# Kernel tuning notes

Measured on AMD Instinct MI355X. Metric: run time of the kernel, lower is better.

The kernel has to match this reference:

```python
import jax, jax.numpy as jnp
import numpy as np

B, N = 8, 8192
S_ATTN, S_NONE = 128, 384          # npoint = (npoint_all=512, npoint_none_attn=384) -> npoint_attn=128
S = S_ATTN + S_NONE
NSAMPLE = 64
RADIUS = 0.4
D_FEAT = 64
MLP = [64, 64, 128]
IN_CH = 3 + D_FEAT


def fps(pts, K):
    # pytorch3d.sample_farthest_points, start index 0, full lengths. pts: [B,N,3]
    B_, N_, _ = pts.shape
    def body(carry, _):
        min_d2, last = carry
        lp = jnp.take_along_axis(pts, last[:, None, None], axis=1)      # [B,1,3]
        d2 = jnp.sum((pts - lp) ** 2, -1)                               # [B,N]
        min_d2 = jnp.minimum(min_d2, d2)
        nxt = jnp.argmax(min_d2, -1).astype(jnp.int32)
        return (min_d2, nxt), last
    init = (jnp.full((B_, N_), jnp.float32(1e10)), jnp.zeros((B_,), jnp.int32))
    _, idxs = jax.lax.scan(body, init, None, length=K)
    idxs = idxs.T                                                       # [B,K]
    sampled = jnp.take_along_axis(pts, idxs[..., None], axis=1)         # [B,K,3]
    return sampled, idxs


def ball_query(query, pts, K, radius):
    # pytorch3d.ball_query: first K points with d2 < r^2 in index order; idx pad=-1, nn pad=0.
    d2 = jnp.sum((query[:, :, None, :] - pts[:, None, :, :]) ** 2, -1)  # [B,S,N]
    mask = d2 < radius * radius
    order = jnp.cumsum(mask.astype(jnp.int32), -1) - 1
    slot = jnp.where(mask & (order < K), order, K)                      # overflow -> dump slot K
    n_ids = jnp.broadcast_to(jnp.arange(pts.shape[1], dtype=jnp.int32), slot.shape)
    def scatter_row(slot_row, ids_row):
        return jnp.full((K + 1,), -1, jnp.int32).at[slot_row].set(ids_row)[:K]
    idx = jax.vmap(jax.vmap(scatter_row))(slot, n_ids)                  # [B,S,K]
    valid = idx >= 0
    gathered = jax.vmap(lambda p, i: p[i])(pts, jnp.where(valid, idx, 0))  # [B,S,K,3]
    nn = jnp.where(valid[..., None], gathered, 0.0)
    return idx, nn


def _forward(xyz, points, attention, ws, bs):
    xyz_t = xyz.transpose(0, 2, 1)            # [B,N,3]
    pts_t = points.transpose(0, 2, 1)         # [B,N,D]
    attn_t = attention.transpose(0, 2, 1)     # [B,N,1]

    attn_xyz = attn_t * xyz_t
    none_xyz = (1.0 - attn_t) * xyz_t
    new_attn_xyz, idx_a = fps(attn_xyz, S_ATTN)
    new_none_xyz, idx_n = fps(none_xyz, S_NONE)
    new_xyz = jnp.concatenate([new_attn_xyz, new_none_xyz], axis=1)     # [B,S,3]
    fps_idx = jnp.concatenate([idx_a, idx_n], axis=1)                   # [B,S]
    new_attention = jnp.take_along_axis(attn_t, fps_idx[..., None], axis=1)  # [B,S,1]

    idx, grouped_xyz = ball_query(new_xyz, xyz_t, NSAMPLE, RADIUS)
    grouped_norm = grouped_xyz - new_xyz[:, :, None, :]                 # [B,S,K,3]
    gather_idx = jnp.where(idx < 0, N - 1, idx)   # torch index -1 wraps to last point
    grouped_pts = jax.vmap(lambda p, i: p[i])(pts_t, gather_idx)        # [B,S,K,D]
    feat = jnp.concatenate([grouped_norm, grouped_pts], -1)             # [B,S,K,3+D]

    x = feat.transpose(0, 3, 2, 1)                                      # [B,C,K,S]
    for w, b in zip(ws, bs):                                            # 1x1 Conv2d + ReLU
        x = jax.nn.relu(jnp.einsum('oc,bcks->boks', w, x) + b[None, :, None, None])
    new_points = jnp.max(x, axis=2)                                     # MaxPool over nsample -> [B,C',S]
    return new_xyz.transpose(0, 2, 1), new_points, new_attention.transpose(0, 2, 1)


def setup_inputs() -> dict:
    key = jax.random.key(0)
    ks = jax.random.split(key, 8)
    xyz = jax.random.normal(ks[0], (B, 3, N), jnp.float32)
    points = jax.random.normal(ks[1], (B, D_FEAT, N), jnp.float32)
    attention = jnp.round(jax.random.uniform(ks[2], (B, 1, N), jnp.float32))  # 0/1 mask
    inp = {'xyz': xyz, 'points': points, 'attention': attention}
    last = IN_CH
    for i, oc in enumerate(MLP):
        inp[f'w{i}'] = jax.random.normal(ks[3 + i], (oc, last), jnp.float32) / np.float32(np.sqrt(last))
        inp[f'b{i}'] = jnp.zeros((oc,), jnp.float32)
        last = oc
    return inp


def reference(xyz, points, attention, w0, b0, w1, b1, w2, b2):
    return _forward(xyz, points, attention, (w0, w1, w2), (b0, b1, b2))
```

## Files before the change

### kernel.cpp

```cpp
#include <hip/hip_runtime.h>
#include <cstdint>
#include <cstddef>

#define NB 8
#define NPTS 8192
#define S_TOT 512
#define NSAMP 64
#define DFEAT 64
#define INCH 67
#define SLOTS 17
#define CCAP (SLOTS * 256)

typedef __attribute__((ext_vector_type(8))) short v8s;
typedef __attribute__((ext_vector_type(4))) short v4s;
typedef __attribute__((ext_vector_type(4))) float v4f;

__device__ __forceinline__ float d2_exact(float ax, float ay, float az,
                                          float bx, float by, float bz) {
    float dx = __fsub_rn(ax, bx);
    float dy = __fsub_rn(ay, by);
    float dz = __fsub_rn(az, bz);
    return __fadd_rn(__fadd_rn(__fmul_rn(dx, dx), __fmul_rn(dy, dy)), __fmul_rn(dz, dz));
}

__device__ __forceinline__ unsigned short f2b(float f) {
    unsigned u = __float_as_uint(f);
    return (unsigned short)((u + 0x7fffu + ((u >> 16) & 1u)) >> 16);
}

template <int CTRL>
__device__ __forceinline__ unsigned long long dpp_max_u64(unsigned long long k) {
    int lo = (int)(unsigned)(k & 0xffffffffull);
    int hi = (int)(unsigned)(k >> 32);
    int slo = __builtin_amdgcn_update_dpp(lo, lo, CTRL, 0xf, 0xf, false);
    int shi = __builtin_amdgcn_update_dpp(hi, hi, CTRL, 0xf, 0xf, false);
    unsigned long long o = ((unsigned long long)(unsigned)shi << 32) | (unsigned)slo;
    return (o > k) ? o : k;
}

__global__ __launch_bounds__(1024) void fps_compact(
    const float* __restrict__ xyz, const float* __restrict__ attn,
    float4* __restrict__ cxyz, int* __restrict__ hdr)
{
    int blk = blockIdx.x;
    int b = blk >> 1, grp = blk & 1;
    const float* xb = xyz + (size_t)b * 3 * NPTS;
    const float* ab = attn + (size_t)b * NPTS;
    float4* c4 = cxyz + (size_t)blk * CCAP;

    int tid = threadIdx.x, lane = tid & 63, wid = tid >> 6;
    int n0 = tid * 8;

    __shared__ int s_repmin;
    __shared__ int s_ws[16];
    if (tid == 0) s_repmin = NPTS;
    __syncthreads();

    float av[8];
    *(float4*)&av[0] = *(const float4*)(ab + n0);
    *(float4*)&av[4] = *(const float4*)(ab + n0 + 4);
    int cnt = 0, mymin = NPTS;
    bool keep[8];
#pragma unroll
    for (int j = 0; j < 8; j++) {
        keep[j] = grp ? (av[j] == 0.0f) : (av[j] != 0.0f);
        cnt += keep[j] ? 1 : 0;
        if (!keep[j] && n0 + j < mymin) mymin = n0 + j;
    }
    if (mymin < NPTS) atomicMin(&s_repmin, mymin);

    int incl = cnt;
#pragma unroll
    for (int off = 1; off <= 32; off <<= 1) {
        int t = __shfl_up(incl, off);
        if (lane >= off) incl += t;
    }
    if (lane == 63) s_ws[wid] = incl;
    __syncthreads();
    int woff = 0, tot = 0;
#pragma unroll
    for (int w = 0; w < 16; w++) { if (w < wid) woff += s_ws[w]; tot += s_ws[w]; }
    int pos = woff + incl - cnt;
    int rm = s_repmin;
    int rm_eff = (rm < NPTS) ? rm : 0x7fffffff;

    float xv[8], yv[8], zv[8];
    *(float4*)&xv[0] = *(const float4*)(xb + n0);
    *(float4*)&xv[4] = *(const float4*)(xb + n0 + 4);
    *(float4*)&yv[0] = *(const float4*)(xb + NPTS + n0);
    *(float4*)&yv[4] = *(const float4*)(xb + NPTS + n0 + 4);
    *(float4*)&zv[0] = *(const float4*)(xb + 2 * NPTS + n0);
    *(float4*)&zv[4] = *(const float4*)(xb + 2 * NPTS + n0 + 4);
#pragma unroll
    for (int j = 0; j < 8; j++) {
        if (keep[j]) {
            int fin = pos + ((n0 + j > rm_eff) ? 1 : 0);
            if (fin < CCAP)
                c4[fin] = make_float4(xv[j], yv[j], zv[j], 0.0f);
            pos++;
        }
    }
    if (tid == 0) {
        int M = tot;
        if (rm < NPTS) {
            if (rm < CCAP)
                c4[rm] = make_float4(__fmul_rn(0.0f, xb[rm]),
                                     __fmul_rn(0.0f, xb[NPTS + rm]),
                                     __fmul_rn(0.0f, xb[2 * NPTS + rm]), 0.0f);
            M++;
        }
        hdr[blk * 2] = M;
        hdr[blk * 2 + 1] = (rm < NPTS) ? rm : -1;
    }
}

__global__ __launch_bounds__(256, 1) void fps_fused(
    const float* __restrict__ attn,
    const float4* __restrict__ cxyz,
    const int* __restrict__ hdr,
    float* __restrict__ out0, float* __restrict__ out2,
    const float* __restrict__ pts, unsigned short* __restrict__ ptsTh,
    const float* __restrict__ w0, const float* __restrict__ w1,
    const float* __restrict__ w2, unsigned short* __restrict__ wp)
{
    __shared__ __align__(16) char smem[69632 + 6144 + 64];
    int blk = blockIdx.x;
    int tid = threadIdx.x;

    if (blk < 16) {
        int b = blk >> 1, grp = blk & 1;
        int K = grp ? 384 : 128;
        int soff = grp ? 128 : 0;
        int M = hdr[blk * 2];
        int repslot = hdr[blk * 2 + 1];
        if (M > CCAP) return;
        int lane = tid & 63, wid = tid >> 6;

        const float4* cb = cxyz + (size_t)blk * CCAP;
        float4* sc = (float4*)smem;
        float4* s_obuf = (float4*)(smem + 69632);
        unsigned long long* s_red = (unsigned long long*)(smem + 69632 + 6144);

        float px[SLOTS], py[SLOTS], pz[SLOTS], md[SLOTS];
#pragma unroll
        for (int i = 0; i < SLOTS; i++) {
            int sl = i * 256 + tid;
            bool v = sl < M;
            float4 c = v ? cb[sl] : make_float4(0.f, 0.f, 0.f, 0.f);
            px[i] = c.x; py[i] = c.y; pz[i] = c.z;
            sc[sl] = c;
            md[i] = v ? 1e10f : -1.0f;
        }
        float4 c0 = cb[0];
        float lx = c0.x, ly = c0.y, lz = c0.z;
        float a_last = attn[(size_t)b * NPTS];
        float kept_a = grp ? 0.0f : 1.0f;
        float rep_a  = grp ? 1.0f : 0.0f;

        for (int k = 0; k < K; k++) {
            if (tid == 0) s_obuf[k] = make_float4(lx, ly, lz, a_last);
            if (k == K - 1) break;

            float bv = -1.0f; int bslot = 0x7fffffff;
#pragma unroll
            for (int i = 0; i < SLOTS; i++) {
                float d2 = d2_exact(px[i], py[i], pz[i], lx, ly, lz);
                md[i] = fminf(md[i], d2);
                int sl = i * 256 + tid;
                bool w = (md[i] > bv) || ((md[i] == bv) && (sl < bslot));
                bv = w ? md[i] : bv;
                bslot = w ? sl : bslot;
            }
            unsigned long long key = (bv >= 0.0f)
                ? (((unsigned long long)__float_as_uint(bv) << 32) | (unsigned)(~bslot))
                : 0ull;
            key = dpp_max_u64<0x111>(key);
            key = dpp_max_u64<0x112>(key);
            key = dpp_max_u64<0x114>(key);
            key = dpp_max_u64<0x118>(key);
            key = dpp_max_u64<0x142>(key);
            key = dpp_max_u64<0x143>(key);
            int buf = k & 1;
            if (lane == 63) s_red[buf * 4 + wid] = key;
            __syncthreads();

            const unsigned long long* rp = &s_red[buf * 4];
            unsigned long long k0 = rp[0], k1 = rp[1], k2 = rp[2], k3 = rp[3];
            unsigned long long m01 = (k0 > k1) ? k0 : k1;
            unsigned long long m23 = (k2 > k3) ? k2 : k3;
            unsigned long long g = (m01 > m23) ? m01 : m23;
            int wslot = (int)(~(unsigned)g);
            float4 wc = sc[wslot];
            lx = wc.x; ly = wc.y; lz = wc.z;
            a_last = (wslot == repslot) ? rep_a : kept_a;
        }
        __syncthreads();
        for (int k2i = tid; k2i < K; k2i += 256) {
            float4 o = s_obuf[k2i];
            int sg = soff + k2i;
            out0[(size_t)b * 3 * S_TOT + sg] = o.x;
            out0[(size_t)b * 3 * S_TOT + S_TOT + sg] = o.y;
            out0[(size_t)b * 3 * S_TOT + 2 * S_TOT + sg] = o.z;
            out2[(size_t)b * S_TOT + sg] = o.w;
        }
    } else if (blk < 16 + 1024) {
        float (*t)[65] = (float(*)[65])smem;
        int blk2 = blk - 16;
        int b = blk2 >> 7;
        int n0 = (blk2 & 127) * 64;
        int tx = tid & 63, ty = tid >> 6;
        for (int c = ty; c < 64; c += 4)
            t[c][tx] = pts[((size_t)b * DFEAT + c) * NPTS + n0 + tx];
        __syncthreads();
        for (int r = ty; r < 64; r += 4)
            ptsTh[((size_t)b * NPTS + n0 + r) * DFEAT + tx] = f2b(t[tx][r]);
    } else if (tid < 64) {
        int t = blk - (16 + 1024), l = tid;
        int kq = (l >> 4) * 8, n16 = l & 15;
        unsigned short o[8];
#pragma unroll
        for (int j = 0; j < 8; j++) {
            float v;
            if (t < 12) {
                int kt = t >> 2, nt = t & 3;
                int k = kt * 32 + kq + j, n = nt * 16 + n16;
                v = (k < 64) ? w0[n * INCH + 3 + k] : (k < 67 ? w0[n * INCH + (k - 64)] : 0.0f);
            } else if (t < 20) {
                int tt = t - 12, kt = tt >> 2, nt = tt & 3;
                v = w1[(nt * 16 + n16) * 64 + kt * 32 + kq + j];
            } else {
                int tt = t - 20, kt = tt >> 3, nt = tt & 7;
                v = w2[(nt * 16 + n16) * 64 + kt * 32 + kq + j];
            }
            o[j] = f2b(v);
        }
        *(v8s*)&wp[(size_t)t * 512 + l * 8] = *(v8s*)o;
    }
}

__global__ __launch_bounds__(1024, 1) void fps_kernel(
    const float* __restrict__ xyz, const float* __restrict__ attn,
    const int* __restrict__ hdr,
    float* __restrict__ out0, float* __restrict__ out2)
{
    int blk = blockIdx.x;
    if (hdr != nullptr && hdr[blk * 2] <= CCAP) return;
    int b = blk >> 1, grp = blk & 1;
    int K = grp ? 384 : 128;
    int soff = grp ? 128 : 0;
    int tid = threadIdx.x, lane = tid & 63, wid = tid >> 6;
    const float* xb = xyz + (size_t)b * 3 * NPTS;
    const float* ab = attn + (size_t)b * NPTS;

    float px[8], py[8], pz[8], md[8];
#pragma unroll
    for (int i = 0; i < 8; i++) {
        int n = tid + i * 1024;
        float a = ab[n];
        float f = grp ? __fsub_rn(1.0f, a) : a;
        px[i] = __fmul_rn(f, xb[n]);
        py[i] = __fmul_rn(f, xb[NPTS + n]);
        pz[i] = __fmul_rn(f, xb[2 * NPTS + n]);
        md[i] = 1e10f;
    }
    __shared__ unsigned long long s_red[2][16];
    float a_last = ab[0];
    float f0 = grp ? __fsub_rn(1.0f, a_last) : a_last;
    float lx = __fmul_rn(f0, xb[0]);
    float ly = __fmul_rn(f0, xb[NPTS]);
    float lz = __fmul_rn(f0, xb[2 * NPTS]);

    for (int k = 0; k < K; k++) {
        if (tid == 0) {
            int sg = soff + k;
            out0[(size_t)b * 3 * S_TOT + sg] = lx;
            out0[(size_t)b * 3 * S_TOT + S_TOT + sg] = ly;
            out0[(size_t)b * 3 * S_TOT + 2 * S_TOT + sg] = lz;
            out2[(size_t)b * S_TOT + sg] = a_last;
        }
        if (k == K - 1) break;
        float bv = -1.0f; int bi = 0;
#pragma unroll
        for (int i = 0; i < 8; i++) {
            float d2 = d2_exact(px[i], py[i], pz[i], lx, ly, lz);
            md[i] = fminf(md[i], d2);
            if (md[i] > bv) { bv = md[i]; bi = tid + i * 1024; }
        }
        unsigned long long best =
            ((unsigned long long)__float_as_uint(bv) << 32) | (unsigned)(~bi);
#pragma unroll
        for (int off = 32; off >= 1; off >>= 1) {
            unsigned long long o = __shfl_down(best, off);
            best = (o > best) ? o : best;
        }
        if (lane == 0) s_red[k & 1][wid] = best;
        __syncthreads();
        unsigned long long r = (lane < 16) ? s_red[k & 1][lane] : 0ull;
#pragma unroll
        for (int off = 8; off >= 1; off >>= 1) {
            unsigned long long o = __shfl_down(r, off);
            r = (o > r) ? o : r;
        }
        r = __shfl(r, 0);
        int n = (int)(~(unsigned)r);
        a_last = ab[n];
        float fl = grp ? __fsub_rn(1.0f, a_last) : a_last;
        lx = __fmul_rn(fl, xb[n]);
        ly = __fmul_rn(fl, xb[NPTS + n]);
        lz = __fmul_rn(fl, xb[2 * NPTS + n]);
    }
}

__global__ __launch_bounds__(64, 2) void ball_mlp_mfma(
    const float* __restrict__ xyz,
    const unsigned short* __restrict__ ptsTh,
    const unsigned short* __restrict__ wp,
    const float* __restrict__ b0, const float* __restrict__ b1,
    const float* __restrict__ b2,
    const float* __restrict__ out0,
    float* __restrict__ out1)
{
    const float R2 = (float)(0.4 * 0.4);
    int q = blockIdx.x;
    int b = q >> 9;
    int sg = q & 511;
    int lane = threadIdx.x;
    int col = lane & 15, quad = lane >> 4, kq = quad * 8;

    const float* xb = xyz + (size_t)b * 3 * NPTS;
    float qx = out0[(size_t)b * 3 * S_TOT + sg];
    float qy = out0[(size_t)b * 3 * S_TOT + S_TOT + sg];
    float qz = out0[(size_t)b * 3 * S_TOT + 2 * S_TOT + sg];

    __shared__ int s_idx[NSAMP];
    __shared__ __align__(16) short sBuf[64 * 104];
    unsigned long long* s_mask = (unsigned long long*)sBuf;

#pragma unroll 8
    for (int j = 0; j < 128; j++) {
        int n = j * 64 + lane;
        float d2 = d2_exact(qx, qy, qz, xb[n], xb[NPTS + n], xb[2 * NPTS + n]);
        unsigned long long m = __ballot(d2 < R2);
        if (lane == 0) s_mask[j] = m;
    }

    unsigned long long m0 = s_mask[lane];
    unsigned long long m1 = s_mask[64 + lane];
    int c0 = (int)__popcll(m0), c1 = (int)__popcll(m1);
    int i0 = c0;
#pragma unroll
    for (int off = 1; off <= 32; off <<= 1) {
        int t = __shfl_up(i0, off);
        if (lane >= off) i0 += t;
    }
    int T0 = __shfl(i0, 63);
    int i1 = c1;
#pragma unroll
    for (int off = 1; off <= 32; off <<= 1) {
        int t = __shfl_up(i1, off);
        if (lane >= off) i1 += t;
    }
    int total = T0 + __shfl(i1, 63);
    int p0 = i0 - c0;
    int p1 = T0 + i1 - c1;

    {
        int base = p0, org = lane * 64;
        while (m0 && base < NSAMP) {
            int bp = __ffsll((long long)m0) - 1;
            s_idx[base++] = org + bp;
            m0 &= m0 - 1;
        }
        base = p1; org = (64 + lane) * 64;
        while (m1 && base < NSAMP) {
            int bp = __ffsll((long long)m1) - 1;
            s_idx[base++] = org + bp;
            m1 &= m1 - 1;
        }
    }
    int cnt = (total > NSAMP) ? NSAMP : total;

    int nb = (lane < cnt) ? s_idx[lane] : -1;
    float nx_ = 0.f, ny_ = 0.f, nz_ = 0.f;
    if (nb >= 0) { nx_ = xb[nb]; ny_ = xb[NPTS + nb]; nz_ = xb[2 * NPTS + nb]; }
    float fx = nx_ - qx, fy = ny_ - qy, fz = nz_ - qz;
    int row = (nb < 0) ? (NPTS - 1) : nb;

    {
        const unsigned short* ph = ptsTh + ((size_t)b * NPTS + row) * DFEAT;
        short* xr = &sBuf[lane * 104];
#pragma unroll
        for (int i = 0; i < 8; i++)
            *(v8s*)(xr + i * 8) = *(const v8s*)(ph + i * 8);
#pragma unroll
        for (int i = 0; i < 5; i++)
            *(v8s*)(xr + 64 + i * 8) = (v8s)0;
        v4s xyzp;
        xyzp[0] = (short)f2b(fx); xyzp[1] = (short)f2b(fy);
        xyzp[2] = (short)f2b(fz); xyzp[3] = 0;
        *(v4s*)(xr + 64) = xyzp;
    }

    const v8s* wpv = (const v8s*)wp;

    v4f acc[4][4];
#pragma unroll
    for (int nt = 0; nt < 4; nt++) {
        float bb = b0[nt * 16 + col];
#pragma unroll
        for (int mt = 0; mt < 4; mt++) acc[mt][nt] = (v4f){bb, bb, bb, bb};
    }
#pragma unroll
    for (int kt = 0; kt < 3; kt++) {
        v8s bf[4];
#pragma unroll
        for (int nt = 0; nt < 4; nt++) bf[nt] = wpv[(kt * 4 + nt) * 64 + lane];
#pragma unroll
        for (int mt = 0; mt < 4; mt++) {
            v8s a = *(const v8s*)&sBuf[(mt * 16 + col) * 104 + kt * 32 + kq];
#pragma unroll
            for (int nt = 0; nt < 4; nt++)
                acc[mt][nt] = __builtin_amdgcn_mfma_f32_16x16x32_bf16(a, bf[nt], acc[mt][nt], 0, 0, 0);
        }
    }
#pragma unroll
    for (int mt = 0; mt < 4; mt++)
#pragma unroll
        for (int nt = 0; nt < 4; nt++)
#pragma unroll
            for (int r = 0; r < 4; r++)
                sBuf[(mt * 16 + quad * 4 + r) * 72 + nt * 16 + col] =
                    (short)f2b(fmaxf(acc[mt][nt][r], 0.0f));

#pragma unroll
    for (int nt = 0; nt < 4; nt++) {
        float bb = b1[nt * 16 + col];
#pragma unroll
        for (int mt = 0; mt < 4; mt++) acc[mt][nt] = (v4f){bb, bb, bb, bb};
    }
#pragma unroll
    for (int kt = 0; kt < 2; kt++) {
        v8s bf[4];
#pragma unroll
        for (int nt = 0; nt < 4; nt++) bf[nt] = wpv[(12 + kt * 4 + nt) * 64 + lane];
#pragma unroll
        for (int mt = 0; mt < 4; mt++) {
            v8s a = *(const v8s*)&sBuf[(mt * 16 + col) * 72 + kt * 32 + kq];
#pragma unroll
            for (int nt = 0; nt < 4; nt++)
                acc[mt][nt] = __builtin_amdgcn_mfma_f32_16x16x32_bf16(a, bf[nt], acc[mt][nt], 0, 0, 0);
        }
    }
#pragma unroll
    for (int mt = 0; mt < 4; mt++)
#pragma unroll
        for (int nt = 0; nt < 4; nt++)
#pragma unroll
            for (int r = 0; r < 4; r++)
                sBuf[(mt * 16 + quad * 4 + r) * 72 + nt * 16 + col] =
                    (short)f2b(fmaxf(acc[mt][nt][r], 0.0f));

#pragma unroll
    for (int p = 0; p < 2; p++) {
#pragma unroll
        for (int nt = 0; nt < 4; nt++) {
            float bb = b2[(p * 4 + nt) * 16 + col];
#pragma unroll
            for (int mt = 0; mt < 4; mt++) acc[mt][nt] = (v4f){bb, bb, bb, bb};
        }
#pragma unroll
        for (int kt = 0; kt < 2; kt++) {
            v8s bf[4];
#pragma unroll
            for (int nt = 0; nt < 4; nt++)
                bf[nt] = wpv[(20 + kt * 8 + p * 4 + nt) * 64 + lane];
#pragma unroll
            for (int mt = 0; mt < 4; mt++) {
                v8s a = *(const v8s*)&sBuf[(mt * 16 + col) * 72 + kt * 32 + kq];
#pragma unroll
                for (int nt = 0; nt < 4; nt++)
                    acc[mt][nt] = __builtin_amdgcn_mfma_f32_16x16x32_bf16(a, bf[nt], acc[mt][nt], 0, 0, 0);
            }
        }
#pragma unroll
        for (int nt = 0; nt < 4; nt++) {
            float v = 0.0f;
#pragma unroll
            for (int mt = 0; mt < 4; mt++)
#pragma unroll
                for (int r = 0; r < 4; r++)
                    v = fmaxf(v, acc[mt][nt][r]);
            v = fmaxf(v, __shfl_xor(v, 16));
            v = fmaxf(v, __shfl_xor(v, 32));
            if (lane < 16)
                out1[((size_t)(b * 128 + (p * 4 + nt) * 16 + lane)) * S_TOT + sg] = v;
        }
    }
}

__global__ __launch_bounds__(64, 1) void ball_mlp_fb(
    const float* __restrict__ xyz, const float* __restrict__ pts,
    const float* __restrict__ w0, const float* __restrict__ b0,
    const float* __restrict__ w1, const float* __restrict__ b1,
    const float* __restrict__ w2, const float* __restrict__ b2,
    const float* __restrict__ out0, float* __restrict__ out1)
{
    const float R2 = (float)(0.4 * 0.4);
    int q = blockIdx.x;
    int b = q >> 9, sg = q & 511, lane = threadIdx.x;
    const float* xb = xyz + (size_t)b * 3 * NPTS;
    float qx = out0[(size_t)b * 3 * S_TOT + sg];
    float qy = out0[(size_t)b * 3 * S_TOT + S_TOT + sg];
    float qz = out0[(size_t)b * 3 * S_TOT + 2 * S_TOT + sg];

    __shared__ int s_idx[NSAMP];
    __shared__ float s_h[32 * 64];
    int cnt = 0;
    for (int base = 0; base < NPTS; base += 64) {
        int n = base + lane;
        float d2 = d2_exact(qx, qy, qz, xb[n], xb[NPTS + n], xb[2 * NPTS + n]);
        bool flag = d2 < R2;
        unsigned long long m = __ballot(flag);
        int pos = cnt + (int)__popcll(m & ((1ull << lane) - 1ull));
        if (flag && pos < NSAMP) s_idx[pos] = n;
        cnt += (int)__popcll(m);
    }
    if (cnt > NSAMP) cnt = NSAMP;
    int nb = (lane < cnt) ? s_idx[lane] : -1;
    float nx_ = 0.f, ny_ = 0.f, nz_ = 0.f;
    if (nb >= 0) { nx_ = xb[nb]; ny_ = xb[NPTS + nb]; nz_ = xb[2 * NPTS + nb]; }
    float fx = nx_ - qx, fy = ny_ - qy, fz = nz_ - qz;
    int row = (nb < 0) ? (NPTS - 1) : nb;

    float h1[64];
#pragma unroll
    for (int o = 0; o < 64; o++) {
        float a = __builtin_fmaf(w0[o * INCH + 0], fx, b0[o]);
        a = __builtin_fmaf(w0[o * INCH + 1], fy, a);
        h1[o] = __builtin_fmaf(w0[o * INCH + 2], fz, a);
    }
    const float* pb = pts + (size_t)b * DFEAT * NPTS + row;
#pragma unroll 1
    for (int c = 0; c < 64; c++) {
        float f = pb[(size_t)c * NPTS];
#pragma unroll
        for (int o = 0; o < 64; o++)
            h1[o] = __builtin_fmaf(w0[o * INCH + 3 + c], f, h1[o]);
    }
#pragma unroll
    for (int c = 0; c < 32; c++) s_h[c * 64 + lane] = fmaxf(h1[c], 0.0f);
    float h1h[32];
#pragma unroll
    for (int c = 0; c < 32; c++) h1h[c] = fmaxf(h1[32 + c], 0.0f);

    float h2[64];
#pragma unroll
    for (int o = 0; o < 64; o++) h2[o] = b1[o];
#pragma unroll 1
    for (int c = 0; c < 32; c++) {
        float hc = s_h[c * 64 + lane];
#pragma unroll
        for (int o = 0; o < 64; o++)
            h2[o] = __builtin_fmaf(w1[o * 64 + c], hc, h2[o]);
    }
#pragma unroll
    for (int c = 0; c < 32; c++) s_h[c * 64 + lane] = h1h[c];
#pragma unroll 1
    for (int c = 0; c < 32; c++) {
        float hc = s_h[c * 64 + lane];
#pragma unroll
        for (int o = 0; o < 64; o++)
            h2[o] = __builtin_fmaf(w1[o * 64 + (32 + c)], hc, h2[o]);
    }
#pragma unroll
    for (int o = 0; o < 64; o++) h2[o] = fmaxf(h2[o], 0.0f);

#pragma unroll 2
    for (int o = 0; o < 128; o++) {
        const float* wr = w2 + o * 64;
        float acc = b2[o];
#pragma unroll
        for (int c = 0; c < 64; c++) acc = __builtin_fmaf(wr[c], h2[c], acc);
        acc = fmaxf(acc, 0.0f);
#pragma unroll
        for (int off = 32; off >= 1; off >>= 1)
            acc = fmaxf(acc, __shfl_down(acc, off));
        if (lane == 0) out1[((size_t)(b * 128 + o)) * S_TOT + sg] = acc;
    }
}

extern "C" void kernel_launch(void* const* d_in, const int* in_sizes, int n_in,
                              void* d_out, int out_size, void* d_ws, size_t ws_size,
                              hipStream_t stream) {
    const float* xyz  = (const float*)d_in[0];
    const float* pts  = (const float*)d_in[1];
    const float* attn = (const float*)d_in[2];
    const float* w0 = (const float*)d_in[3];
    const float* b0 = (const float*)d_in[4];
    const float* w1 = (const float*)d_in[5];
    const float* b1 = (const float*)d_in[6];
    const float* w2 = (const float*)d_in[7];
    const float* b2 = (const float*)d_in[8];

    float* out0 = (float*)d_out;
    float* out1 = out0 + (size_t)NB * 3 * S_TOT;
    float* out2 = out1 + (size_t)NB * 128 * S_TOT;

    unsigned short* wp    = (unsigned short*)d_ws;
    unsigned short* ptsTh = (unsigned short*)((char*)d_ws + 36864);
    float4*         cxyz  = (float4*)((char*)d_ws + 36864 + 8388608);
    int*            hdr   = (int*)((char*)cxyz + (size_t)16 * CCAP * 16);
    const size_t need = 36864 + 8388608 + (size_t)16 * CCAP * 16 + 128;

    if (ws_size >= need) {
        fps_compact<<<16, 1024, 0, stream>>>(xyz, attn, cxyz, hdr);
        fps_fused<<<16 + 1024 + 36, 256, 0, stream>>>(
            attn, cxyz, hdr, out0, out2, pts, ptsTh, w0, w1, w2, wp);
        fps_kernel<<<16, 1024, 0, stream>>>(xyz, attn, hdr, out0, out2);
        ball_mlp_mfma<<<NB * S_TOT, 64, 0, stream>>>(xyz, ptsTh, wp, b0, b1, b2,
                                                     out0, out1);
    } else {
        fps_kernel<<<16, 1024, 0, stream>>>(xyz, attn, nullptr, out0, out2);
        ball_mlp_fb<<<NB * S_TOT, 64, 0, stream>>>(xyz, pts, w0, b0, w1, b1,
                                                   w2, b2, out0, out1);
    }
}
```

Baseline: 630.7 us.

## Overlap ball-query MLP with FPS via progress flags in fused kernel

Appends 1024 consumer blocks to the fused FPS kernel. FPS blocks publish sampled centroids every 16 iterations through release fences and per-block progress counters. Consumer warps spin on those counters and on a transpose/weight-pack completion count, then run ball query plus the MFMA MLP for their centroid while FPS continues. A timeout marks queries as skipped so a tail kernel recomputes them, which guards against deadlock when consumers cannot be co-resident with producers, at the cost of spin-wait overhead and raised FPS wave priority.

```diff
diff --git a/kernel.cpp b/kernel.cpp
--- a/kernel.cpp
+++ b/kernel.cpp
@@ -10,6 +10,8 @@
 #define INCH 67
 #define SLOTS 17
 #define CCAP (SLOTS * 256)
+#define TDONE 1060
+#define BALLW 13568
 
 typedef __attribute__((ext_vector_type(8))) short v8s;
 typedef __attribute__((ext_vector_type(4))) short v4s;
@@ -38,17 +40,205 @@
     return (o > k) ? o : k;
 }
 
+__device__ __forceinline__ void ball_one(
+    const float* __restrict__ xyz,
+    const unsigned short* __restrict__ ptsTh,
+    const unsigned short* __restrict__ wp,
+    const float* __restrict__ b0, const float* __restrict__ b1,
+    const float* __restrict__ b2,
+    const float* __restrict__ out0, float* __restrict__ out1,
+    int b, int sg, int lane, short* sBuf, int* s_idx)
+{
+    const float R2 = (float)(0.4 * 0.4);
+    int col = lane & 15, quad = lane >> 4, kq = quad * 8;
+
+    const float* xb = xyz + (size_t)b * 3 * NPTS;
+    float qx = out0[(size_t)b * 3 * S_TOT + sg];
+    float qy = out0[(size_t)b * 3 * S_TOT + S_TOT + sg];
+    float qz = out0[(size_t)b * 3 * S_TOT + 2 * S_TOT + sg];
+
+    unsigned long long* s_mask = (unsigned long long*)sBuf;
+
+#pragma unroll 8
+    for (int j = 0; j < 128; j++) {
+        int n = j * 64 + lane;
+        float d2 = d2_exact(qx, qy, qz, xb[n], xb[NPTS + n], xb[2 * NPTS + n]);
+        unsigned long long m = __ballot(d2 < R2);
+        if (lane == 0) s_mask[j] = m;
+    }
+
+    unsigned long long m0 = s_mask[lane];
+    unsigned long long m1 = s_mask[64 + lane];
+    int c0 = (int)__popcll(m0), c1 = (int)__popcll(m1);
+    int i0 = c0;
+#pragma unroll
+    for (int off = 1; off <= 32; off <<= 1) {
+        int t = __shfl_up(i0, off);
+        if (lane >= off) i0 += t;
+    }
+    int T0 = __shfl(i0, 63);
+    int i1 = c1;
+#pragma unroll
+    for (int off = 1; off <= 32; off <<= 1) {
+        int t = __shfl_up(i1, off);
+        if (lane >= off) i1 += t;
+    }
+    int total = T0 + __shfl(i1, 63);
+    int p0 = i0 - c0;
+    int p1 = T0 + i1 - c1;
+
+    {
+        int base = p0, org = lane * 64;
+        while (m0 && base < NSAMP) {
+            int bp = __ffsll((long long)m0) - 1;
+            s_idx[base++] = org + bp;
+            m0 &= m0 - 1;
+        }
+        base = p1; org = (64 + lane) * 64;
+        while (m1 && base < NSAMP) {
+            int bp = __ffsll((long long)m1) - 1;
+            s_idx[base++] = org + bp;
+            m1 &= m1 - 1;
+        }
+    }
+    int cnt = (total > NSAMP) ? NSAMP : total;
+
+    int nb = (lane < cnt) ? s_idx[lane] : -1;
+    float nx_ = 0.f, ny_ = 0.f, nz_ = 0.f;
+    if (nb >= 0) { nx_ = xb[nb]; ny_ = xb[NPTS + nb]; nz_ = xb[2 * NPTS + nb]; }
+    float fx = nx_ - qx, fy = ny_ - qy, fz = nz_ - qz;
+    int row = (nb < 0) ? (NPTS - 1) : nb;
+
+    {
+        const unsigned short* ph = ptsTh + ((size_t)b * NPTS + row) * DFEAT;
+        short* xr = &sBuf[lane * 104];
+#pragma unroll
+        for (int i = 0; i < 8; i++)
+            *(v8s*)(xr + i * 8) = *(const v8s*)(ph + i * 8);
+#pragma unroll
+        for (int i = 0; i < 5; i++)
+            *(v8s*)(xr + 64 + i * 8) = (v8s)0;
+        v4s xyzp;
+        xyzp[0] = (short)f2b(fx); xyzp[1] = (short)f2b(fy);
+        xyzp[2] = (short)f2b(fz); xyzp[3] = 0;
+        *(v4s*)(xr + 64) = xyzp;
+    }
+
+    const v8s* wpv = (const v8s*)wp;
+
+    v4f acc[4][4];
+#pragma unroll
+    for (int nt = 0; nt < 4; nt++) {
+        float bb = b0[nt * 16 + col];
+#pragma unroll
+        for (int mt = 0; mt < 4; mt++) acc[mt][nt] = (v4f){bb, bb, bb, bb};
+    }
+#pragma unroll
+    for (int kt = 0; kt < 3; kt++) {
+        v8s bf[4];
+#pragma unroll
+        for (int nt = 0; nt < 4; nt++) bf[nt] = wpv[(kt * 4 + nt) * 64 + lane];
+#pragma unroll
+        for (int mt = 0; mt < 4; mt++) {
+            v8s a = *(const v8s*)&sBuf[(mt * 16 + col) * 104 + kt * 32 + kq];
+#pragma unroll
+            for (int nt = 0; nt < 4; nt++)
+                acc[mt][nt] = __builtin_amdgcn_mfma_f32_16x16x32_bf16(a, bf[nt], acc[mt][nt], 0, 0, 0);
+        }
+    }
+#pragma unroll
+    for (int mt = 0; mt < 4; mt++)
+#pragma unroll
+        for (int nt = 0; nt < 4; nt++)
+#pragma unroll
+            for (int r = 0; r < 4; r++)
+                sBuf[(mt * 16 + quad * 4 + r) * 72 + nt * 16 + col] =
+                    (short)f2b(fmaxf(acc[mt][nt][r], 0.0f));
+
+#pragma unroll
+    for (int nt = 0; nt < 4; nt++) {
+        float bb = b1[nt * 16 + col];
+#pragma unroll
+        for (int mt = 0; mt < 4; mt++) acc[mt][nt] = (v4f){bb, bb, bb, bb};
+    }
+#pragma unroll
+    for (int kt = 0; kt < 2; kt++) {
+        v8s bf[4];
+#pragma unroll
+        for (int nt = 0; nt < 4; nt++) bf[nt] = wpv[(12 + kt * 4 + nt) * 64 + lane];
+#pragma unroll
+        for (int mt = 0; mt < 4; mt++) {
+            v8s a = *(const v8s*)&sBuf[(mt * 16 + col) * 72 + kt * 32 + kq];
+#pragma unroll
+            for (int nt = 0; nt < 4; nt++)
+                acc[mt][nt] = __builtin_amdgcn_mfma_f32_16x16x32_bf16(a, bf[nt], acc[mt][nt], 0, 0, 0);
+        }
+    }
+#pragma unroll
+    for (int mt = 0; mt < 4; mt++)
+#pragma unroll
+        for (int nt = 0; nt < 4; nt++)
+#pragma unroll
+            for (int r = 0; r < 4; r++)
+                sBuf[(mt * 16 + quad * 4 + r) * 72 + nt * 16 + col] =
+                    (short)f2b(fmaxf(acc[mt][nt][r], 0.0f));
+
+#pragma unroll
+    for (int p = 0; p < 2; p++) {
+#pragma unroll
+        for (int nt = 0; nt < 4; nt++) {
+            float bb = b2[(p * 4 + nt) * 16 + col];
+#pragma unroll
+            for (int mt = 0; mt < 4; mt++) acc[mt][nt] = (v4f){bb, bb, bb, bb};
+        }
+#pragma unroll
+        for (int kt = 0; kt < 2; kt++) {
+            v8s bf[4];
+#pragma unroll
+            for (int nt = 0; nt < 4; nt++)
+                bf[nt] = wpv[(20 + kt * 8 + p * 4 + nt) * 64 + lane];
+#pragma unroll
+            for (int mt = 0; mt < 4; mt++) {
+                v8s a = *(const v8s*)&sBuf[(mt * 16 + col) * 72 + kt * 32 + kq];
+#pragma unroll
+                for (int nt = 0; nt < 4; nt++)
+                    acc[mt][nt] = __builtin_amdgcn_mfma_f32_16x16x32_bf16(a, bf[nt], acc[mt][nt], 0, 0, 0);
+            }
+        }
+#pragma unroll
+        for (int nt = 0; nt < 4; nt++) {
+            float v = 0.0f;
+#pragma unroll
+            for (int mt = 0; mt < 4; mt++)
+#pragma unroll
+                for (int r = 0; r < 4; r++)
+                    v = fmaxf(v, acc[mt][nt][r]);
+            v = fmaxf(v, __shfl_xor(v, 16));
+            v = fmaxf(v, __shfl_xor(v, 32));
+            if (lane < 16)
+                out1[((size_t)(b * 128 + (p * 4 + nt) * 16 + lane)) * S_TOT + sg] = v;
+        }
+    }
+}
+
 __global__ __launch_bounds__(1024) void fps_compact(
     const float* __restrict__ xyz, const float* __restrict__ attn,
-    float4* __restrict__ cxyz, int* __restrict__ hdr)
+    float4* __restrict__ cxyz, int* __restrict__ hdr,
+    int* __restrict__ prog, int* __restrict__ tcount, int* __restrict__ skip)
 {
     int blk = blockIdx.x;
+    int tid = threadIdx.x;
+    if (blk == 0) {
+        if (tid < 16) prog[tid] = 0;
+        if (tid == 16) tcount[0] = 0;
+        ((int4*)skip)[tid] = make_int4(0, 0, 0, 0);
+    }
     int b = blk >> 1, grp = blk & 1;
     const float* xb = xyz + (size_t)b * 3 * NPTS;
     const float* ab = attn + (size_t)b * NPTS;
     float4* c4 = cxyz + (size_t)blk * CCAP;
 
-    int tid = threadIdx.x, lane = tid & 63, wid = tid >> 6;
+    int lane = tid & 63, wid = tid >> 6;
     int n0 = tid * 8;
 
     __shared__ int s_repmin;
@@ -121,7 +311,12 @@
     float* __restrict__ out0, float* __restrict__ out2,
     const float* __restrict__ pts, unsigned short* __restrict__ ptsTh,
     const float* __restrict__ w0, const float* __restrict__ w1,
-    const float* __restrict__ w2, unsigned short* __restrict__ wp)
+    const float* __restrict__ w2, unsigned short* __restrict__ wp,
+    const float* __restrict__ xyz,
+    const float* __restrict__ b0v, const float* __restrict__ b1v,
+    const float* __restrict__ b2v,
+    float* __restrict__ out1,
+    int* __restrict__ prog, int* __restrict__ tcount, int* __restrict__ skip)
 {
     __shared__ __align__(16) char smem[69632 + 6144 + 64];
     int blk = blockIdx.x;
@@ -133,8 +328,13 @@
         int soff = grp ? 128 : 0;
         int M = hdr[blk * 2];
         int repslot = hdr[blk * 2 + 1];
-        if (M > CCAP) return;
+        if (M > CCAP) {
+            if (tid == 0)
+                __hip_atomic_store(&prog[blk], -1, __ATOMIC_RELAXED, __HIP_MEMORY_SCOPE_AGENT);
+            return;
+        }
         int lane = tid & 63, wid = tid >> 6;
+        __builtin_amdgcn_s_setprio(1);
 
         const float4* cb = cxyz + (size_t)blk * CCAP;
         float4* sc = (float4*)smem;
@@ -193,15 +393,38 @@
             float4 wc = sc[wslot];
             lx = wc.x; ly = wc.y; lz = wc.z;
             a_last = (wslot == repslot) ? rep_a : kept_a;
+
+            if (((k & 15) == 15) && wid == 3) {
+                if (lane < 16) {
+                    int kk = k - 15 + lane;
+                    float4 o = s_obuf[kk];
+                    int sgO = soff + kk;
+                    size_t base = (size_t)b * 3 * S_TOT;
+                    out0[base + sgO] = o.x;
+                    out0[base + S_TOT + sgO] = o.y;
+                    out0[base + 2 * S_TOT + sgO] = o.z;
+                    out2[(size_t)b * S_TOT + sgO] = o.w;
+                }
+                __builtin_amdgcn_fence(__ATOMIC_RELEASE, "agent");
+                if (lane == 0)
+                    __hip_atomic_store(&prog[blk], k + 1, __ATOMIC_RELAXED, __HIP_MEMORY_SCOPE_AGENT);
+            }
         }
         __syncthreads();
-        for (int k2i = tid; k2i < K; k2i += 256) {
-            float4 o = s_obuf[k2i];
-            int sg = soff + k2i;
-            out0[(size_t)b * 3 * S_TOT + sg] = o.x;
-            out0[(size_t)b * 3 * S_TOT + S_TOT + sg] = o.y;
-            out0[(size_t)b * 3 * S_TOT + 2 * S_TOT + sg] = o.z;
-            out2[(size_t)b * S_TOT + sg] = o.w;
+        if (wid == 3) {
+            if (lane < 16) {
+                int kk = K - 16 + lane;
+                float4 o = s_obuf[kk];
+                int sgO = soff + kk;
+                size_t base = (size_t)b * 3 * S_TOT;
+                out0[base + sgO] = o.x;
+                out0[base + S_TOT + sgO] = o.y;
+                out0[base + 2 * S_TOT + sgO] = o.z;
+                out2[(size_t)b * S_TOT + sgO] = o.w;
+            }
+            __builtin_amdgcn_fence(__ATOMIC_RELEASE, "agent");
+            if (lane == 0)
+                __hip_atomic_store(&prog[blk], K, __ATOMIC_RELAXED, __HIP_MEMORY_SCOPE_AGENT);
         }
     } else if (blk < 16 + 1024) {
         float (*t)[65] = (float(*)[65])smem;
@@ -214,27 +437,68 @@
         __syncthreads();
         for (int r = ty; r < 64; r += 4)
             ptsTh[((size_t)b * NPTS + n0 + r) * DFEAT + tx] = f2b(t[tx][r]);
-    } else if (tid < 64) {
-        int t = blk - (16 + 1024), l = tid;
-        int kq = (l >> 4) * 8, n16 = l & 15;
-        unsigned short o[8];
-#pragma unroll
-        for (int j = 0; j < 8; j++) {
-            float v;
-            if (t < 12) {
-                int kt = t >> 2, nt = t & 3;
-                int k = kt * 32 + kq + j, n = nt * 16 + n16;
-                v = (k < 64) ? w0[n * INCH + 3 + k] : (k < 67 ? w0[n * INCH + (k - 64)] : 0.0f);
-            } else if (t < 20) {
-                int tt = t - 12, kt = tt >> 2, nt = tt & 3;
-                v = w1[(nt * 16 + n16) * 64 + kt * 32 + kq + j];
-            } else {
-                int tt = t - 20, kt = tt >> 3, nt = tt & 7;
-                v = w2[(nt * 16 + n16) * 64 + kt * 32 + kq + j];
+        __syncthreads();
+        if (tid == 0) {
+            __builtin_amdgcn_fence(__ATOMIC_RELEASE, "agent");
+            __hip_atomic_fetch_add(tcount, 1, __ATOMIC_RELAXED, __HIP_MEMORY_SCOPE_AGENT);
+        }
+    } else if (blk < 1076) {
+        if (tid < 64) {
+            int t = blk - (16 + 1024), l = tid;
+            int kq = (l >> 4) * 8, n16 = l & 15;
+            unsigned short o[8];
+#pragma unroll
+            for (int j = 0; j < 8; j++) {
+                float v;
+                if (t < 12) {
+                    int kt = t >> 2, nt = t & 3;
+                    int k = kt * 32 + kq + j, n = nt * 16 + n16;
+                    v = (k < 64) ? w0[n * INCH + 3 + k] : (k < 67 ? w0[n * INCH + (k - 64)] : 0.0f);
+                } else if (t < 20) {
+                    int tt = t - 12, kt = tt >> 2, nt = tt & 3;
+                    v = w1[(nt * 16 + n16) * 64 + kt * 32 + kq + j];
+                } else {
+                    int tt = t - 20, kt = tt >> 3, nt = tt & 7;
+                    v = w2[(nt * 16 + n16) * 64 + kt * 32 + kq + j];
+                }
+                o[j] = f2b(v);
             }
-            o[j] = f2b(v);
-        }
-        *(v8s*)&wp[(size_t)t * 512 + l * 8] = *(v8s*)o;
+            *(v8s*)&wp[(size_t)t * 512 + l * 8] = *(v8s*)o;
+        }
+        if (tid == 0) {
+            __builtin_amdgcn_fence(__ATOMIC_RELEASE, "agent");
+            __hip_atomic_fetch_add(tcount, 1, __ATOMIC_RELAXED, __HIP_MEMORY_SCOPE_AGENT);
+        }
+    } else {
+        int lane = tid & 63, wid = tid >> 6;
+        int w = (blk - 1076) * 4 + wid;
+        int b, grp, kk;
+        if (w < 2048) { kk = w >> 4; int r = w & 15; b = r & 7; grp = r >> 3; }
+        else          { int w2 = w - 2048; kk = 128 + (w2 >> 3); b = w2 & 7; grp = 1; }
+        int sg = (grp ? 128 : 0) + kk;
+        int q = b * 512 + sg;
+        int pblk = b * 2 + grp;
+
+        int ok = 1;
+        for (int to = 0;;) {
+            int p = __hip_atomic_load(&prog[pblk], __ATOMIC_RELAXED, __HIP_MEMORY_SCOPE_AGENT);
+            if (p < 0) { ok = 0; break; }
+            if (p > kk) {
+                int t = __hip_atomic_load(tcount, __ATOMIC_RELAXED, __HIP_MEMORY_SCOPE_AGENT);
+                if (t >= TDONE) break;
+            }
+            if (++to > 500) { ok = 0; break; }
+            __builtin_amdgcn_s_sleep(64);
+        }
+        if (!ok) {
+            if (lane == 0) skip[q] = 1;
+            return;
+        }
+        __builtin_amdgcn_fence(__ATOMIC_ACQUIRE, "agent");
+
+        short* sBufW = (short*)(smem + wid * BALLW);
+        int* s_idxW = (int*)(smem + wid * BALLW + 13312);
+        ball_one(xyz, ptsTh, wp, b0v, b1v, b2v, out0, out1, b, sg, lane, sBufW, s_idxW);
     }
 }
 
@@ -311,191 +575,23 @@
     }
 }
 
-__global__ __launch_bounds__(64, 2) void ball_mlp_mfma(
+__global__ __launch_bounds__(256) void ball_tail(
     const float* __restrict__ xyz,
     const unsigned short* __restrict__ ptsTh,
     const unsigned short* __restrict__ wp,
     const float* __restrict__ b0, const float* __restrict__ b1,
     const float* __restrict__ b2,
-    const float* __restrict__ out0,
-    float* __restrict__ out1)
+    const float* __restrict__ out0, float* __restrict__ out1,
+    const int* __restrict__ skip)
 {
-    const float R2 = (float)(0.4 * 0.4);
-    int q = blockIdx.x;
-    int b = q >> 9;
-    int sg = q & 511;
-    int lane = threadIdx.x;
-    int col = lane & 15, quad = lane >> 4, kq = quad * 8;
-
-    const float* xb = xyz + (size_t)b * 3 * NPTS;
-    float qx = out0[(size_t)b * 3 * S_TOT + sg];
-    float qy = out0[(size_t)b * 3 * S_TOT + S_TOT + sg];
-    float qz = out0[(size_t)b * 3 * S_TOT + 2 * S_TOT + sg];
-
-    __shared__ int s_idx[NSAMP];
-    __shared__ __align__(16) short sBuf[64 * 104];
-    unsigned long long* s_mask = (unsigned long long*)sBuf;
-
-#pragma unroll 8
-    for (int j = 0; j < 128; j++) {
-        int n = j * 64 + lane;
-        float d2 = d2_exact(qx, qy, qz, xb[n], xb[NPTS + n], xb[2 * NPTS + n]);
-        unsigned long long m = __ballot(d2 < R2);
-        if (lane == 0) s_mask[j] = m;
-    }
-
-    unsigned long long m0 = s_mask[lane];
-    unsigned long long m1 = s_mask[64 + lane];
-    int c0 = (int)__popcll(m0), c1 = (int)__popcll(m1);
-    int i0 = c0;
-#pragma unroll
-    for (int off = 1; off <= 32; off <<= 1) {
-        int t = __shfl_up(i0, off);
-        if (lane >= off) i0 += t;
-    }
-    int T0 = __shfl(i0, 63);
-    int i1 = c1;
-#pragma unroll
-    for (int off = 1; off <= 32; off <<= 1) {
-        int t = __shfl_up(i1, off);
-        if (lane >= off) i1 += t;
-    }
-    int total = T0 + __shfl(i1, 63);
-    int p0 = i0 - c0;
-    int p1 = T0 + i1 - c1;
-
-    {
-        int base = p0, org = lane * 64;
-        while (m0 && base < NSAMP) {
-            int bp = __ffsll((long long)m0) - 1;
-            s_idx[base++] = org + bp;
-            m0 &= m0 - 1;
-        }
-        base = p1; org = (64 + lane) * 64;
-        while (m1 && base < NSAMP) {
-            int bp = __ffsll((long long)m1) - 1;
-            s_idx[base++] = org + bp;
-            m1 &= m1 - 1;
-        }
-    }
-    int cnt = (total > NSAMP) ? NSAMP : total;
-
-    int nb = (lane < cnt) ? s_idx[lane] : -1;
-    float nx_ = 0.f, ny_ = 0.f, nz_ = 0.f;
-    if (nb >= 0) { nx_ = xb[nb]; ny_ = xb[NPTS + nb]; nz_ = xb[2 * NPTS + nb]; }
-    float fx = nx_ - qx, fy = ny_ - qy, fz = nz_ - qz;
-    int row = (nb < 0) ? (NPTS - 1) : nb;
-
-    {
-        const unsigned short* ph = ptsTh + ((size_t)b * NPTS + row) * DFEAT;
-        short* xr = &sBuf[lane * 104];
-#pragma unroll
-        for (int i = 0; i < 8; i++)
-            *(v8s*)(xr + i * 8) = *(const v8s*)(ph + i * 8);
-#pragma unroll
-        for (int i = 0; i < 5; i++)
-            *(v8s*)(xr + 64 + i * 8) = (v8s)0;
-        v4s xyzp;
-        xyzp[0] = (short)f2b(fx); xyzp[1] = (short)f2b(fy);
-        xyzp[2] = (short)f2b(fz); xyzp[3] = 0;
-        *(v4s*)(xr + 64) = xyzp;
-    }
-
-    const v8s* wpv = (const v8s*)wp;
-
-    v4f acc[4][4];
-#pragma unroll
-    for (int nt = 0; nt < 4; nt++) {
-        float bb = b0[nt * 16 + col];
-#pragma unroll
-        for (int mt = 0; mt < 4; mt++) acc[mt][nt] = (v4f){bb, bb, bb, bb};
-    }
-#pragma unroll
-    for (int kt = 0; kt < 3; kt++) {
-        v8s bf[4];
-#pragma unroll
-        for (int nt = 0; nt < 4; nt++) bf[nt] = wpv[(kt * 4 + nt) * 64 + lane];
-#pragma unroll
-        for (int mt = 0; mt < 4; mt++) {
-            v8s a = *(const v8s*)&sBuf[(mt * 16 + col) * 104 + kt * 32 + kq];
-#pragma unroll
-            for (int nt = 0; nt < 4; nt++)
-                acc[mt][nt] = __builtin_amdgcn_mfma_f32_16x16x32_bf16(a, bf[nt], acc[mt][nt], 0, 0, 0);
-        }
-    }
-#pragma unroll
-    for (int mt = 0; mt < 4; mt++)
-#pragma unroll
-        for (int nt = 0; nt < 4; nt++)
-#pragma unroll
-            for (int r = 0; r < 4; r++)
-                sBuf[(mt * 16 + quad * 4 + r) * 72 + nt * 16 + col] =
-                    (short)f2b(fmaxf(acc[mt][nt][r], 0.0f));
-
-#pragma unroll
-    for (int nt = 0; nt < 4; nt++) {
-        float bb = b1[nt * 16 + col];
-#pragma unroll
-        for (int mt = 0; mt < 4; mt++) acc[mt][nt] = (v4f){bb, bb, bb, bb};
-    }
-#pragma unroll
-    for (int kt = 0; kt < 2; kt++) {
-        v8s bf[4];
-#pragma unroll
-        for (int nt = 0; nt < 4; nt++) bf[nt] = wpv[(12 + kt * 4 + nt) * 64 + lane];
-#pragma unroll
-        for (int mt = 0; mt < 4; mt++) {
-            v8s a = *(const v8s*)&sBuf[(mt * 16 + col) * 72 + kt * 32 + kq];
-#pragma unroll
-            for (int nt = 0; nt < 4; nt++)
-                acc[mt][nt] = __builtin_amdgcn_mfma_f32_16x16x32_bf16(a, bf[nt], acc[mt][nt], 0, 0, 0);
-        }
-    }
-#pragma unroll
-    for (int mt = 0; mt < 4; mt++)
-#pragma unroll
-        for (int nt = 0; nt < 4; nt++)
-#pragma unroll
-            for (int r = 0; r < 4; r++)
-                sBuf[(mt * 16 + quad * 4 + r) * 72 + nt * 16 + col] =
-                    (short)f2b(fmaxf(acc[mt][nt][r], 0.0f));
-
-#pragma unroll
-    for (int p = 0; p < 2; p++) {
-#pragma unroll
-        for (int nt = 0; nt < 4; nt++) {
-            float bb = b2[(p * 4 + nt) * 16 + col];
-#pragma unroll
-            for (int mt = 0; mt < 4; mt++) acc[mt][nt] = (v4f){bb, bb, bb, bb};
-        }
-#pragma unroll
-        for (int kt = 0; kt < 2; kt++) {
-            v8s bf[4];
-#pragma unroll
-            for (int nt = 0; nt < 4; nt++)
-                bf[nt] = wpv[(20 + kt * 8 + p * 4 + nt) * 64 + lane];
-#pragma unroll
-            for (int mt = 0; mt < 4; mt++) {
-                v8s a = *(const v8s*)&sBuf[(mt * 16 + col) * 72 + kt * 32 + kq];
-#pragma unroll
-                for (int nt = 0; nt < 4; nt++)
-                    acc[mt][nt] = __builtin_amdgcn_mfma_f32_16x16x32_bf16(a, bf[nt], acc[mt][nt], 0, 0, 0);
-            }
-        }
-#pragma unroll
-        for (int nt = 0; nt < 4; nt++) {
-            float v = 0.0f;
-#pragma unroll
-            for (int mt = 0; mt < 4; mt++)
-#pragma unroll
-                for (int r = 0; r < 4; r++)
-                    v = fmaxf(v, acc[mt][nt][r]);
-            v = fmaxf(v, __shfl_xor(v, 16));
-            v = fmaxf(v, __shfl_xor(v, 32));
-            if (lane < 16)
-                out1[((size_t)(b * 128 + (p * 4 + nt) * 16 + lane)) * S_TOT + sg] = v;
-        }
-    }
+    __shared__ __align__(16) char smem[4 * BALLW];
+    int lane = threadIdx.x & 63, wid = threadIdx.x >> 6;
+    int q = blockIdx.x * 4 + wid;
+    if (skip[q] == 0) return;
+    int b = q >> 9, sg = q & 511;
+    short* sBufW = (short*)(smem + wid * BALLW);
+    int* s_idxW = (int*)(smem + wid * BALLW + 13312);
+    ball_one(xyz, ptsTh, wp, b0, b1, b2, out0, out1, b, sg, lane, sBufW, s_idxW);
 }
 
 __global__ __launch_bounds__(64, 1) void ball_mlp_fb(
@@ -610,15 +706,20 @@
     unsigned short* ptsTh = (unsigned short*)((char*)d_ws + 36864);
     float4*         cxyz  = (float4*)((char*)d_ws + 36864 + 8388608);
     int*            hdr   = (int*)((char*)cxyz + (size_t)16 * CCAP * 16);
-    const size_t need = 36864 + 8388608 + (size_t)16 * CCAP * 16 + 128;
+    int*            prog  = hdr + 32;
+    int*            tcnt  = prog + 16;
+    int*            skip  = tcnt + 4;
+    const size_t need = 36864 + 8388608 + (size_t)16 * CCAP * 16 + 128
+                        + (16 + 4 + 4096) * 4 + 64;
 
     if (ws_size >= need) {
-        fps_compact<<<16, 1024, 0, stream>>>(xyz, attn, cxyz, hdr);
-        fps_fused<<<16 + 1024 + 36, 256, 0, stream>>>(
-            attn, cxyz, hdr, out0, out2, pts, ptsTh, w0, w1, w2, wp);
+        fps_compact<<<16, 1024, 0, stream>>>(xyz, attn, cxyz, hdr, prog, tcnt, skip);
+        fps_fused<<<16 + 1024 + 36 + 1024, 256, 0, stream>>>(
+            attn, cxyz, hdr, out0, out2, pts, ptsTh, w0, w1, w2, wp,
+            xyz, b0, b1, b2, out1, prog, tcnt, skip);
         fps_kernel<<<16, 1024, 0, stream>>>(xyz, attn, hdr, out0, out2);
-        ball_mlp_mfma<<<NB * S_TOT, 64, 0, stream>>>(xyz, ptsTh, wp, b0, b1, b2,
-                                                     out0, out1);
+        ball_tail<<<1024, 256, 0, stream>>>(xyz, ptsTh, wp, b0, b1, b2,
+                                            out0, out1, skip);
     } else {
         fps_kernel<<<16, 1024, 0, stream>>>(xyz, attn, nullptr, out0, out2);
         ball_mlp_fb<<<NB * S_TOT, 64, 0, stream>>>(xyz, pts, w0, b0, w1, b1,
```

Result: faster. 606.1 us (-3.9%).
